# Optimization experiments

Hardware: AMD Instinct MI355X
Metric: run time of the kernel (lower is better)

The kernel has to match this reference:

```python
import jax, jax.numpy as jnp
import numpy as np

B, C, IC, H, W = 2, 64, 32, 96, 96


def setup_inputs() -> dict:
    key = jax.random.key(0)
    ks = jax.random.split(key, 8)
    s_in = 1.0 / np.sqrt(C)
    s_ic = 1.0 / np.sqrt(IC)
    return {
        "x": jax.random.normal(ks[0], (B, C, H, W), dtype=jnp.float32),
        "Wg": jax.random.uniform(ks[1], (IC, C), jnp.float32, -s_in, s_in),
        "bg": jax.random.uniform(ks[2], (IC,), jnp.float32, -s_in, s_in),
        "Wt": jax.random.uniform(ks[3], (IC, C), jnp.float32, -s_in, s_in),
        "bt": jax.random.uniform(ks[4], (IC,), jnp.float32, -s_in, s_in),
        "Wp": jax.random.uniform(ks[5], (IC, C), jnp.float32, -s_in, s_in),
        "bp": jax.random.uniform(ks[6], (IC,), jnp.float32, -s_in, s_in),
        "Wo": jax.random.uniform(ks[7], (C, IC), jnp.float32, -s_ic, s_ic),
        "bo": jax.random.uniform(jax.random.fold_in(key, 9), (C,), jnp.float32, -s_ic, s_ic),
    }


def reference(x, Wg, bg, Wt, bt, Wp, bp, Wo, bo):
    b, c, h, w = x.shape
    n = h * w
    xf = x.reshape(b, c, n)  # [B, C, N]

    def proj(Wc, bc):  # 1x1 conv == channel GEMM -> [B, IC, N]
        return jnp.einsum("bcn,oc->bon", xf, Wc) + bc[None, :, None]

    g = proj(Wg, bg)
    theta = proj(Wt, bt)
    phi = proj(Wp, bp)
    scores = jnp.einsum("bcn,bcm->bnm", theta, phi)  # [B, N, N]
    att = jax.nn.softmax(scores, axis=-1)
    y = jnp.einsum("bnm,bcm->bcn", att, g)  # [B, IC, N]
    o = jnp.einsum("bcn,oc->bon", y, Wo) + bo[None, :, None]  # [B, C, N]
    return o.reshape(b, c, h, w) + x
```

## Files before the change

kernel.cpp:

```cpp
#include <hip/hip_runtime.h>
#include <hip/hip_bf16.h>


#define B_   2
#define C_   64
#define IC_  32
#define N_   9216
#define SEG_       4
#define SEG_KEYS   2304
#define SEG_TILES  36
#define QBLKS      144
#define LOG2E 1.44269504088896f

typedef __attribute__((ext_vector_type(4))) float  f32x4;
typedef __attribute__((ext_vector_type(8))) short  s16x8;
typedef __attribute__((ext_vector_type(4))) short  s16x4;

static __device__ __forceinline__ ushort f2bf(float f) {
  union { __hip_bfloat16 h; ushort u; } cv;
  cv.h = __float2bfloat16(f);
  return cv.u;
}

static __device__ __forceinline__ f32x4 mfma32(s16x8 a, s16x8 b, f32x4 c) {
  return __builtin_amdgcn_mfma_f32_16x16x32_bf16(a, b, c, 0, 0, 0);
}

__global__ __launch_bounds__(256) void proj_kernel(
    const float* __restrict__ x,
    const float* __restrict__ Wg, const float* __restrict__ bg,
    const float* __restrict__ Wt, const float* __restrict__ bt,
    const float* __restrict__ Wp, const float* __restrict__ bp,
    ushort* __restrict__ Qb, ushort* __restrict__ Kb, ushort* __restrict__ Vt)
{
  const int g    = blockIdx.x / 18;
  const int nblk = blockIdx.x % 18;
  const int bn0  = nblk * 1024 + threadIdx.x * 4;
  const int b    = bn0 / N_;
  const int n    = bn0 % N_;

  float ag[4], at_[4], ap[4];
#pragma unroll
  for (int j = 0; j < 4; ++j) { ag[j] = 0.f; at_[j] = 0.f; ap[j] = 0.f; }

  const float* xp = x + (size_t)b * C_ * N_ + n;
#pragma unroll 8
  for (int c = 0; c < C_; ++c) {
    const f32x4 x0 = *reinterpret_cast<const f32x4*>(xp + (size_t)c * N_);
    const float wg = Wg[g * C_ + c];
    const float wt = Wt[g * C_ + c];
    const float wp = Wp[g * C_ + c];
#pragma unroll
    for (int j = 0; j < 4; ++j) {
      ag[j]  = fmaf(wg, x0[j], ag[j]);
      at_[j] = fmaf(wt, x0[j], at_[j]);
      ap[j]  = fmaf(wp, x0[j], ap[j]);
    }
  }

  const float bgv = bg[g], btv = bt[g], bpv = bp[g];
  union { ushort u[4]; s16x4 v; } vt4;
#pragma unroll
  for (int j = 0; j < 4; ++j) {
    const int bn = bn0 + j;
    Qb[(size_t)bn * IC_ + g] = f2bf(LOG2E * (at_[j] + btv));
    Kb[(size_t)bn * IC_ + g] = f2bf(ap[j] + bpv);
    vt4.u[j] = f2bf(ag[j] + bgv);
  }
  *reinterpret_cast<s16x4*>(Vt + (size_t)(b * IC_ + g) * N_ + n) = vt4.v;
}

__global__ __launch_bounds__(256) void attn_kernel(
    const ushort* __restrict__ Qb, const ushort* __restrict__ Kb,
    const ushort* __restrict__ Vt, float* __restrict__ Opart,
    float* __restrict__ Lp)
{
  __shared__ __align__(16) ushort Kl[64 * 40];
  __shared__ __align__(16) ushort Vl[32 * 68];

  const int qblk = blockIdx.x % QBLKS;
  const int bs   = blockIdx.x / QBLKS;
  const int seg  = bs & (SEG_ - 1);
  const int b    = bs >> 2;
  const int key0 = seg * SEG_KEYS;

  const int tid  = threadIdx.x;
  const int lane = tid & 63;
  const int wave = tid >> 6;
  const int q16  = lane & 15;
  const int h    = lane >> 4;

  const int qbase = qblk * 64 + wave * 16;

  const s16x8 qfrag = *reinterpret_cast<const s16x8*>(
      Qb + (size_t)(b * N_ + qbase + q16) * IC_ + h * 8);

  f32x4 acc0 = {0.f, 0.f, 0.f, 0.f};
  f32x4 acc1 = {0.f, 0.f, 0.f, 0.f};
  float l_run = 0.f;

  const int krow = tid >> 2, kpart = tid & 3;
  const ushort* kg = Kb + ((size_t)b * N_ + key0 + krow) * IC_ + kpart * 8;
  ushort* kl_dst = &Kl[krow * 40 + kpart * 8];

  const int vd0 = tid >> 4, vp = tid & 15;
  const int vd1 = vd0 + 16;
  const ushort* vg0 = Vt + (size_t)(b * IC_ + vd0) * N_ + key0 + vp * 4;
  const ushort* vg1 = Vt + (size_t)(b * IC_ + vd1) * N_ + key0 + vp * 4;
  ushort* vl_dst0 = &Vl[vd0 * 68 + vp * 4];
  ushort* vl_dst1 = &Vl[vd1 * 68 + vp * 4];

  s16x8 kreg = *reinterpret_cast<const s16x8*>(kg);
  s16x4 vreg0 = *reinterpret_cast<const s16x4*>(vg0);
  s16x4 vreg1 = *reinterpret_cast<const s16x4*>(vg1);

  for (int it = 0; it < SEG_TILES; ++it) {
    *reinterpret_cast<s16x8*>(kl_dst)  = kreg;
    *reinterpret_cast<s16x4*>(vl_dst0) = vreg0;
    *reinterpret_cast<s16x4*>(vl_dst1) = vreg1;
    __syncthreads();

    if (it + 1 < SEG_TILES) {
      const int nk = (it + 1) * 64;
      kreg  = *reinterpret_cast<const s16x8*>(kg + (size_t)nk * IC_);
      vreg0 = *reinterpret_cast<const s16x4*>(vg0 + nk);
      vreg1 = *reinterpret_cast<const s16x4*>(vg1 + nk);
    }

    float sc[4][4];
#pragma unroll
    for (int t = 0; t < 4; ++t) {
      const s16x8 kf = *reinterpret_cast<const s16x8*>(&Kl[(t * 16 + q16) * 40 + h * 8]);
      f32x4 z = {0.f, 0.f, 0.f, 0.f};
      const f32x4 st = mfma32(kf, qfrag, z);
      sc[t][0] = st[0]; sc[t][1] = st[1]; sc[t][2] = st[2]; sc[t][3] = st[3];
    }

    float ts = 0.f;
#pragma unroll
    for (int u = 0; u < 2; ++u) {
      union { ushort us[8]; s16x8 v; } pa;
#pragma unroll
      for (int i = 0; i < 4; ++i) {
        const float e0 = __builtin_amdgcn_exp2f(sc[2 * u][i]);
        const float e1 = __builtin_amdgcn_exp2f(sc[2 * u + 1][i]);
        ts += e0 + e1;
        pa.us[i]     = f2bf(e0);
        pa.us[4 + i] = f2bf(e1);
      }
      union { s16x4 q4[2]; s16x8 v; } vf0, vf1;
      vf0.q4[0] = *reinterpret_cast<const s16x4*>(&Vl[q16 * 68 + u * 32 + h * 4]);
      vf0.q4[1] = *reinterpret_cast<const s16x4*>(&Vl[q16 * 68 + u * 32 + 16 + h * 4]);
      vf1.q4[0] = *reinterpret_cast<const s16x4*>(&Vl[(16 + q16) * 68 + u * 32 + h * 4]);
      vf1.q4[1] = *reinterpret_cast<const s16x4*>(&Vl[(16 + q16) * 68 + u * 32 + 16 + h * 4]);
      acc0 = mfma32(pa.v, vf0.v, acc0);
      acc1 = mfma32(pa.v, vf1.v, acc1);
    }
    l_run += ts;
    __syncthreads();
  }

  l_run += __shfl_xor(l_run, 16);
  l_run += __shfl_xor(l_run, 32);

  const size_t obase0 = ((size_t)(b * SEG_ + seg) * N_);
#pragma unroll
  for (int r = 0; r < 4; ++r) {
    const int q = qbase + h * 4 + r;
    Opart[(obase0 + q) * IC_ + q16]      = acc0[r];
    Opart[(obase0 + q) * IC_ + 16 + q16] = acc1[r];
  }
  if (h == 0) {
    Lp[obase0 + qbase + q16] = l_run;
  }
}

__global__ __launch_bounds__(256) void combine_kernel(
    const float* __restrict__ Opart, const float* __restrict__ Lp,
    float* __restrict__ Y)
{
  const int idx  = blockIdx.x * 256 + threadIdx.x;
  const int bn   = idx >> 1;
  const int half = idx & 1;
  const int b    = bn / N_;
  const int q    = bn % N_;

  float l = 0.f;
  f32x4 o0 = {0.f,0.f,0.f,0.f}, o1 = {0.f,0.f,0.f,0.f},
        o2 = {0.f,0.f,0.f,0.f}, o3 = {0.f,0.f,0.f,0.f};
#pragma unroll
  for (int s = 0; s < SEG_; ++s) {
    const size_t base = (size_t)(b * SEG_ + s) * N_ + q;
    l += Lp[base];
    const f32x4* op = reinterpret_cast<const f32x4*>(Opart + base * IC_ + half * 16);
    o0 += op[0]; o1 += op[1]; o2 += op[2]; o3 += op[3];
  }
  const float inv = 1.0f / l;
  f32x4* yp = reinterpret_cast<f32x4*>(Y + (size_t)bn * IC_ + half * 16);
  yp[0] = o0 * inv; yp[1] = o1 * inv; yp[2] = o2 * inv; yp[3] = o3 * inv;
}

__global__ __launch_bounds__(256) void out_kernel(
    const float* __restrict__ Y, const float* __restrict__ Wo,
    const float* __restrict__ bo, const float* __restrict__ x,
    float* __restrict__ out)
{
  const int g    = blockIdx.x / 72;
  const int nblk = blockIdx.x % 72;
  const int bn   = nblk * 256 + threadIdx.x;
  const int b    = bn / N_;
  const int n    = bn % N_;

  float yv[32];
#pragma unroll
  for (int i = 0; i < 8; ++i) {
    const f32x4 v = *reinterpret_cast<const f32x4*>(Y + (size_t)bn * IC_ + i * 4);
    yv[i * 4 + 0] = v[0]; yv[i * 4 + 1] = v[1];
    yv[i * 4 + 2] = v[2]; yv[i * 4 + 3] = v[3];
  }

  float acc[8];
#pragma unroll
  for (int j = 0; j < 8; ++j) acc[j] = bo[g * 8 + j];

#pragma unroll
  for (int ic = 0; ic < IC_; ++ic) {
    const float yv_ic = yv[ic];
#pragma unroll
    for (int j = 0; j < 8; ++j)
      acc[j] = fmaf(Wo[(g * 8 + j) * IC_ + ic], yv_ic, acc[j]);
  }

#pragma unroll
  for (int j = 0; j < 8; ++j) {
    const int oc = g * 8 + j;
    const size_t xi = (size_t)(b * C_ + oc) * N_ + n;
    out[xi] = acc[j] + x[xi];
  }
}

extern "C" void kernel_launch(void* const* d_in, const int* in_sizes, int n_in,
                              void* d_out, int out_size, void* d_ws, size_t ws_size,
                              hipStream_t stream)
{
  const float* x  = (const float*)d_in[0];
  const float* Wg = (const float*)d_in[1];
  const float* bg = (const float*)d_in[2];
  const float* Wt = (const float*)d_in[3];
  const float* bt = (const float*)d_in[4];
  const float* Wp = (const float*)d_in[5];
  const float* bp = (const float*)d_in[6];
  const float* Wo = (const float*)d_in[7];
  const float* bo = (const float*)d_in[8];
  float* out = (float*)d_out;

  char* ws = (char*)d_ws;
  const size_t szb = (size_t)B_ * N_ * IC_ * sizeof(ushort);
  const size_t szy = (size_t)B_ * N_ * IC_ * sizeof(float);
  ushort* Qb = (ushort*)(ws);
  ushort* Kb = (ushort*)(ws + szb);
  ushort* Vt = (ushort*)(ws + 2 * szb);
  float*  Yw = (float*)(ws + 3 * szb);
  float*  Op = (float*)(ws + 3 * szb + szy);
  float*  Lp = (float*)(ws + 3 * szb + szy + (size_t)SEG_ * szy);

  proj_kernel<<<576, 256, 0, stream>>>(x, Wg, bg, Wt, bt, Wp, bp, Qb, Kb, Vt);
  attn_kernel<<<B_ * SEG_ * QBLKS, 256, 0, stream>>>(Qb, Kb, Vt, Op, Lp);
  combine_kernel<<<(B_ * N_ * 2) / 256, 256, 0, stream>>>(Op, Lp, Yw);
  out_kernel<<<576, 256, 0, stream>>>(Yw, Wo, bo, x, out);
}
```

Baseline: 71.77 us.

## Double key-split segments, compute row sums via MFMA, store partials in bf16

Splits the keys into 8 segments instead of 4, doubling the attention grid so more CUs have blocks to run. The softmax denominator is now accumulated by an extra MFMA against a ones vector instead of scalar adds and shuffles. Partial outputs are stored as bf16 to halve combine traffic, combine uses 4 threads per row, and out_kernel uses 4 channels per block with twice as many blocks. Y now reuses the Q buffer region, and the bf16 partials plus the doubled combine work add precision loss and more partial traffic.

```diff
diff --git a/kernel.cpp b/kernel.cpp
--- a/kernel.cpp
+++ b/kernel.cpp
@@ -6,9 +6,9 @@
 #define C_   64
 #define IC_  32
 #define N_   9216
-#define SEG_       4
-#define SEG_KEYS   2304
-#define SEG_TILES  36
+#define SEG_       8
+#define SEG_KEYS   1152
+#define SEG_TILES  18
 #define QBLKS      144
 #define LOG2E 1.44269504088896f
 
@@ -20,6 +20,12 @@
   union { __hip_bfloat16 h; ushort u; } cv;
   cv.h = __float2bfloat16(f);
   return cv.u;
+}
+
+static __device__ __forceinline__ float bf2f(ushort u) {
+  union { uint i; float f; } c;
+  c.i = ((uint)u) << 16;
+  return c.f;
 }
 
 static __device__ __forceinline__ f32x4 mfma32(s16x8 a, s16x8 b, f32x4 c) {
@@ -72,7 +78,7 @@
 
 __global__ __launch_bounds__(256) void attn_kernel(
     const ushort* __restrict__ Qb, const ushort* __restrict__ Kb,
-    const ushort* __restrict__ Vt, float* __restrict__ Opart,
+    const ushort* __restrict__ Vt, ushort* __restrict__ Opart,
     float* __restrict__ Lp)
 {
   __shared__ __align__(16) ushort Kl[64 * 40];
@@ -81,7 +87,7 @@
   const int qblk = blockIdx.x % QBLKS;
   const int bs   = blockIdx.x / QBLKS;
   const int seg  = bs & (SEG_ - 1);
-  const int b    = bs >> 2;
+  const int b    = bs >> 3;
   const int key0 = seg * SEG_KEYS;
 
   const int tid  = threadIdx.x;
@@ -92,12 +98,15 @@
 
   const int qbase = qblk * 64 + wave * 16;
 
+  const short ONE = (short)0x3F80;
+  const s16x8 ones = {ONE, ONE, ONE, ONE, ONE, ONE, ONE, ONE};
+
   const s16x8 qfrag = *reinterpret_cast<const s16x8*>(
       Qb + (size_t)(b * N_ + qbase + q16) * IC_ + h * 8);
 
   f32x4 acc0 = {0.f, 0.f, 0.f, 0.f};
   f32x4 acc1 = {0.f, 0.f, 0.f, 0.f};
-  float l_run = 0.f;
+  f32x4 accL = {0.f, 0.f, 0.f, 0.f};
 
   const int krow = tid >> 2, kpart = tid & 3;
   const ushort* kg = Kb + ((size_t)b * N_ + key0 + krow) * IC_ + kpart * 8;
@@ -136,17 +145,13 @@
       sc[t][0] = st[0]; sc[t][1] = st[1]; sc[t][2] = st[2]; sc[t][3] = st[3];
     }
 
-    float ts = 0.f;
 #pragma unroll
     for (int u = 0; u < 2; ++u) {
       union { ushort us[8]; s16x8 v; } pa;
 #pragma unroll
       for (int i = 0; i < 4; ++i) {
-        const float e0 = __builtin_amdgcn_exp2f(sc[2 * u][i]);
-        const float e1 = __builtin_amdgcn_exp2f(sc[2 * u + 1][i]);
-        ts += e0 + e1;
-        pa.us[i]     = f2bf(e0);
-        pa.us[4 + i] = f2bf(e1);
+        pa.us[i]     = f2bf(__builtin_amdgcn_exp2f(sc[2 * u][i]));
+        pa.us[4 + i] = f2bf(__builtin_amdgcn_exp2f(sc[2 * u + 1][i]));
       }
       union { s16x4 q4[2]; s16x8 v; } vf0, vf1;
       vf0.q4[0] = *reinterpret_cast<const s16x4*>(&Vl[q16 * 68 + u * 32 + h * 4]);
@@ -155,49 +160,54 @@
       vf1.q4[1] = *reinterpret_cast<const s16x4*>(&Vl[(16 + q16) * 68 + u * 32 + 16 + h * 4]);
       acc0 = mfma32(pa.v, vf0.v, acc0);
       acc1 = mfma32(pa.v, vf1.v, acc1);
-    }
-    l_run += ts;
+      accL = mfma32(pa.v, ones,  accL);
+    }
     __syncthreads();
   }
-
-  l_run += __shfl_xor(l_run, 16);
-  l_run += __shfl_xor(l_run, 32);
 
   const size_t obase0 = ((size_t)(b * SEG_ + seg) * N_);
 #pragma unroll
   for (int r = 0; r < 4; ++r) {
     const int q = qbase + h * 4 + r;
-    Opart[(obase0 + q) * IC_ + q16]      = acc0[r];
-    Opart[(obase0 + q) * IC_ + 16 + q16] = acc1[r];
-  }
-  if (h == 0) {
-    Lp[obase0 + qbase + q16] = l_run;
+    Opart[(obase0 + q) * IC_ + q16]      = f2bf(acc0[r]);
+    Opart[(obase0 + q) * IC_ + 16 + q16] = f2bf(acc1[r]);
+  }
+  if (q16 == 0) {
+#pragma unroll
+    for (int r = 0; r < 4; ++r)
+      Lp[obase0 + qbase + h * 4 + r] = accL[r];
   }
 }
 
 __global__ __launch_bounds__(256) void combine_kernel(
-    const float* __restrict__ Opart, const float* __restrict__ Lp,
+    const ushort* __restrict__ Opart, const float* __restrict__ Lp,
     float* __restrict__ Y)
 {
-  const int idx  = blockIdx.x * 256 + threadIdx.x;
-  const int bn   = idx >> 1;
-  const int half = idx & 1;
-  const int b    = bn / N_;
-  const int q    = bn % N_;
+  const int idx     = blockIdx.x * 256 + threadIdx.x;
+  const int bn      = idx >> 2;
+  const int quarter = idx & 3;
+  const int b       = bn / N_;
+  const int q       = bn % N_;
 
   float l = 0.f;
-  f32x4 o0 = {0.f,0.f,0.f,0.f}, o1 = {0.f,0.f,0.f,0.f},
-        o2 = {0.f,0.f,0.f,0.f}, o3 = {0.f,0.f,0.f,0.f};
+  float o[8];
+#pragma unroll
+  for (int j = 0; j < 8; ++j) o[j] = 0.f;
+
 #pragma unroll
   for (int s = 0; s < SEG_; ++s) {
     const size_t base = (size_t)(b * SEG_ + s) * N_ + q;
     l += Lp[base];
-    const f32x4* op = reinterpret_cast<const f32x4*>(Opart + base * IC_ + half * 16);
-    o0 += op[0]; o1 += op[1]; o2 += op[2]; o3 += op[3];
+    union { s16x8 v; ushort us[8]; } ov;
+    ov.v = *reinterpret_cast<const s16x8*>(Opart + base * IC_ + quarter * 8);
+#pragma unroll
+    for (int j = 0; j < 8; ++j) o[j] += bf2f(ov.us[j]);
   }
   const float inv = 1.0f / l;
-  f32x4* yp = reinterpret_cast<f32x4*>(Y + (size_t)bn * IC_ + half * 16);
-  yp[0] = o0 * inv; yp[1] = o1 * inv; yp[2] = o2 * inv; yp[3] = o3 * inv;
+  f32x4 y0 = {o[0] * inv, o[1] * inv, o[2] * inv, o[3] * inv};
+  f32x4 y1 = {o[4] * inv, o[5] * inv, o[6] * inv, o[7] * inv};
+  f32x4* yp = reinterpret_cast<f32x4*>(Y + (size_t)bn * IC_ + quarter * 8);
+  yp[0] = y0; yp[1] = y1;
 }
 
 __global__ __launch_bounds__(256) void out_kernel(
@@ -219,21 +229,21 @@
     yv[i * 4 + 2] = v[2]; yv[i * 4 + 3] = v[3];
   }
 
-  float acc[8];
-#pragma unroll
-  for (int j = 0; j < 8; ++j) acc[j] = bo[g * 8 + j];
+  float acc[4];
+#pragma unroll
+  for (int j = 0; j < 4; ++j) acc[j] = bo[g * 4 + j];
 
 #pragma unroll
   for (int ic = 0; ic < IC_; ++ic) {
     const float yv_ic = yv[ic];
 #pragma unroll
-    for (int j = 0; j < 8; ++j)
-      acc[j] = fmaf(Wo[(g * 8 + j) * IC_ + ic], yv_ic, acc[j]);
-  }
-
-#pragma unroll
-  for (int j = 0; j < 8; ++j) {
-    const int oc = g * 8 + j;
+    for (int j = 0; j < 4; ++j)
+      acc[j] = fmaf(Wo[(g * 4 + j) * IC_ + ic], yv_ic, acc[j]);
+  }
+
+#pragma unroll
+  for (int j = 0; j < 4; ++j) {
+    const int oc = g * 4 + j;
     const size_t xi = (size_t)(b * C_ + oc) * N_ + n;
     out[xi] = acc[j] + x[xi];
   }
@@ -255,17 +265,17 @@
   float* out = (float*)d_out;
 
   char* ws = (char*)d_ws;
-  const size_t szb = (size_t)B_ * N_ * IC_ * sizeof(ushort);
-  const size_t szy = (size_t)B_ * N_ * IC_ * sizeof(float);
+  const size_t szb  = (size_t)B_ * N_ * IC_ * sizeof(ushort);
+  const size_t szOp = (size_t)B_ * SEG_ * N_ * IC_ * sizeof(ushort);
   ushort* Qb = (ushort*)(ws);
   ushort* Kb = (ushort*)(ws + szb);
   ushort* Vt = (ushort*)(ws + 2 * szb);
-  float*  Yw = (float*)(ws + 3 * szb);
-  float*  Op = (float*)(ws + 3 * szb + szy);
-  float*  Lp = (float*)(ws + 3 * szb + szy + (size_t)SEG_ * szy);
+  ushort* Op = (ushort*)(ws + 3 * szb);
+  float*  Lp = (float*)(ws + 3 * szb + szOp);
+  float*  Yw = (float*)(ws);
 
   proj_kernel<<<576, 256, 0, stream>>>(x, Wg, bg, Wt, bt, Wp, bp, Qb, Kb, Vt);
   attn_kernel<<<B_ * SEG_ * QBLKS, 256, 0, stream>>>(Qb, Kb, Vt, Op, Lp);
-  combine_kernel<<<(B_ * N_ * 2) / 256, 256, 0, stream>>>(Op, Lp, Yw);
-  out_kernel<<<576, 256, 0, stream>>>(Yw, Wo, bo, x, out);
-}
+  combine_kernel<<<(B_ * N_ * 4) / 256, 256, 0, stream>>>(Op, Lp, Yw);
+  out_kernel<<<16 * 72, 256, 0, stream>>>(Yw, Wo, bo, x, out);
+}
```

After: 71.75 us. Within noise of the previous version (-0.0%).
